# Optimization experiments

Measured on AMD Instinct MI355X. Metric: run time of the kernel, lower is better.

Reference implementation:

```python
import jax, jax.numpy as jnp
import numpy as np

B, F, D_IN, H, HEADS, NC = 2048, 64, 32, 128, 4, 16
EPG = 128            # random intra-graph edges per graph
N = B * F            # 131072 nodes
E = B * EPG          # 262144 edges (self-loops added in reference, like PyG GATConv)
LRELU_ATT = 0.2      # PyG GATConv negative_slope
LRELU_CLS = 0.01     # nn.LeakyReLU default


def setup_inputs() -> dict:
    key = jax.random.key(0)
    ks = jax.random.split(key, 24)
    emb = jax.random.normal(ks[0], (B, F, D_IN), jnp.float32)
    # per-graph random connectivity, offset so graphs are disjoint
    src_l = jax.random.randint(ks[1], (B, EPG), 0, F)
    tgt_l = jax.random.randint(ks[2], (B, EPG), 0, F)
    off = (jnp.arange(B) * F)[:, None]
    edge_index = jnp.stack([(src_l + off).reshape(-1), (tgt_l + off).reshape(-1)]).astype(jnp.int32)
    batch_idx = jnp.repeat(jnp.arange(B), F).astype(jnp.int32)
    s = 0.05
    return {
        'emb': emb, 'edge_index': edge_index, 'batch_idx': batch_idx,
        # fused aligner (single unique dim 32)
        'W_align': s * jax.random.normal(ks[3], (D_IN, H), jnp.float32),
        'b_align': jnp.zeros((H,), jnp.float32),
        'gate_logits': jnp.full((F,), 2.2, jnp.float32),
        # GATConv 1: in=H, out=H per head, heads=4, concat
        'W1': s * jax.random.normal(ks[4], (H, HEADS * H), jnp.float32),
        'a_src1': s * jax.random.normal(ks[5], (HEADS, H), jnp.float32),
        'a_dst1': s * jax.random.normal(ks[6], (HEADS, H), jnp.float32),
        'b1': jnp.zeros((HEADS * H,), jnp.float32),
        # GATConv 2: in=HEADS*H, out=H, heads=1, concat=False
        'W2': s * jax.random.normal(ks[7], (HEADS * H, H), jnp.float32),
        'a_src2': s * jax.random.normal(ks[8], (1, H), jnp.float32),
        'a_dst2': s * jax.random.normal(ks[9], (1, H), jnp.float32),
        'b2': jnp.zeros((H,), jnp.float32),
        # classifier MLP
        'Wc1': s * jax.random.normal(ks[10], (H, H // 2), jnp.float32),
        'bc1': jnp.zeros((H // 2,), jnp.float32),
        'Wc2': s * jax.random.normal(ks[11], (H // 2, NC), jnp.float32),
        'bc2': jnp.zeros((NC,), jnp.float32),
    }


def gat_layer(x, src, tgt, W, a_src, a_dst, b, concat):
    heads, dout = a_src.shape
    n = x.shape[0]
    h = (x @ W).reshape(n, heads, dout)                       # [N,h,d]
    e = jax.nn.leaky_relu(jnp.einsum('nhd,hd->nh', h, a_src)[src]
                          + jnp.einsum('nhd,hd->nh', h, a_dst)[tgt], LRELU_ATT)  # [E,h]
    m = jax.ops.segment_max(e, tgt, num_segments=n)           # segment softmax over in-neighbors
    p = jnp.exp(e - m[tgt])
    ssum = jax.ops.segment_sum(p, tgt, num_segments=n)
    alpha = p / (ssum[tgt] + 1e-16)
    out = jax.ops.segment_sum(h[src] * alpha[:, :, None], tgt, num_segments=n)
    out = out.reshape(n, heads * dout) if concat else out.mean(axis=1)
    return out + b


def reference(emb, edge_index, batch_idx, W_align, b_align, gate_logits,
              W1, a_src1, a_dst1, b1, W2, a_src2, a_dst2, b2, Wc1, bc1, Wc2, bc2):
    n = emb.shape[0] * emb.shape[1]
    aligned = emb @ W_align + b_align                         # fused align: [B,F,H]
    gate = jax.nn.sigmoid(gate_logits)                        # [F]
    x = (aligned * gate[None, :, None]).reshape(n, -1)        # gated node features [N,H]
    # add self-loops (GATConv default), eval mode -> dropout is identity
    loops = jnp.arange(n, dtype=edge_index.dtype)
    src = jnp.concatenate([edge_index[0], loops])
    tgt = jnp.concatenate([edge_index[1], loops])
    x = gat_layer(x, src, tgt, W1, a_src1, a_dst1, b1, True)  # [N, 4*H]
    x = jax.nn.elu(x)
    x = gat_layer(x, src, tgt, W2, a_src2, a_dst2, b2, False) # [N, H]
    gsum = jax.ops.segment_sum(x, batch_idx, num_segments=B)  # global_mean_pool
    cnt = jax.ops.segment_sum(jnp.ones((n, 1), x.dtype), batch_idx, num_segments=B)
    g = gsum / cnt                                            # [B, H]
    hc = jax.nn.leaky_relu(g @ Wc1 + bc1, LRELU_CLS)
    logits = hc @ Wc2 + bc2                                   # [B, NC]
    return logits, gate
```

## Files before the change

### kernel.cpp

```cpp
#include <hip/hip_runtime.h>
#include <math.h>

#define BLK 256

constexpr int Bg    = 2048;
constexpr int Fn    = 64;
constexpr int DIN   = 32;
constexpr int Hd    = 128;
constexpr int HEADS = 4;
constexpr int NC    = 16;
constexpr int EPG   = 128;
constexpr int Etot  = Bg * EPG;
constexpr int W1C   = HEADS * Hd;
constexpr int NSTR  = 68;
constexpr int EROW  = 136;
constexpr int PROW  = 68;
constexpr int NE    = EPG + Fn;

typedef __attribute__((ext_vector_type(8))) __bf16 bf16x8;
typedef __attribute__((ext_vector_type(4))) __bf16 bf16x4;
typedef __attribute__((ext_vector_type(4))) float  f32x4;

__device__ __align__(16) __bf16 g_wcombT[W1C * DIN];
__device__ float g_c1[W1C];
__device__ float g_c1s[16];
__device__ __align__(16) __bf16 g_w1F[HEADS*8*64*8];
__device__ __align__(16) __bf16 g_w2F[HEADS*4*8*64*8];
__device__ __align__(16) __bf16 g_wscF[HEADS*4*64*8];
__device__ __align__(16) __bf16 g_bs1F[64*8];

__global__ __launch_bounds__(BLK) void prep1(
    const float* __restrict__ Wa, const float* __restrict__ ba,
    const float* __restrict__ W1)
{
  __shared__ float WaS[DIN * Hd];
  const int tid = threadIdx.x;
  for (int i = tid; i < DIN * Hd; i += BLK) {
    int k = i >> 7, m = i & 127;
    WaS[m * DIN + k] = Wa[i];
  }
  __syncthreads();

  int i = blockIdx.x * BLK + tid;
  if (i < DIN * W1C) {
    int k = i & 31, n = i >> 5;
    float a0 = 0.f, a1 = 0.f, a2 = 0.f, a3 = 0.f;
    #pragma unroll
    for (int m = 0; m < Hd; m += 4) {
      a0 += WaS[(m  )*DIN + k] * W1[(m  )*W1C + n];
      a1 += WaS[(m+1)*DIN + k] * W1[(m+1)*W1C + n];
      a2 += WaS[(m+2)*DIN + k] * W1[(m+2)*W1C + n];
      a3 += WaS[(m+3)*DIN + k] * W1[(m+3)*W1C + n];
    }
    g_wcombT[i] = (__bf16)(a0 + a1 + a2 + a3);
  } else if (i < DIN*W1C + W1C) {
    int n = i - DIN*W1C;
    float a0 = 0.f, a1 = 0.f, a2 = 0.f, a3 = 0.f;
    #pragma unroll
    for (int m = 0; m < Hd; m += 4) {
      a0 += ba[m  ] * W1[(m  )*W1C + n];
      a1 += ba[m+1] * W1[(m+1)*W1C + n];
      a2 += ba[m+2] * W1[(m+2)*W1C + n];
      a3 += ba[m+3] * W1[(m+3)*W1C + n];
    }
    g_c1[n] = a0 + a1 + a2 + a3;
  }
}

constexpr int R_W2F  = 65536;
constexpr int R_W1F  = 16384;
constexpr int R_WSCZ = 8192;
constexpr int R_WSCD = 4096;
constexpr int R_BS1Z = 512;
constexpr int R_BS1D = 1024;
constexpr int R_C1S  = 128;
constexpr int B0 = R_W2F;
constexpr int B1 = B0 + R_W1F;
constexpr int B2 = B1 + R_WSCZ;
constexpr int B3 = B2 + R_WSCD;
constexpr int B4 = B3 + R_BS1Z;
constexpr int B5 = B4 + R_BS1D;
constexpr int P2_TOT = B5 + R_C1S;

__global__ __launch_bounds__(BLK) void prep2(
    const float* __restrict__ W2,
    const float* __restrict__ as1, const float* __restrict__ ad1,
    const float* __restrict__ as2, const float* __restrict__ ad2)
{
  int i = blockIdx.x * BLK + threadIdx.x;
  if (i < B0) {
    int k = i >> 7, n = i & 127;
    int hh = k >> 7, Ks = (k >> 5) & 3, q = (k >> 3) & 3, j = k & 7;
    int Nt = n >> 4, l = n & 15;
    int idx = (((hh*4 + Ks)*8 + Nt)*64 + (q*16 + l))*8 + j;
    g_w2F[idx] = (__bf16)W2[i];
  } else if (i < B1) {
    int j = i - B0;
    int jj = j & 7, lane = (j >> 3) & 63, T = j >> 9;
    int hh = T >> 3, Nt = T & 7;
    int q = lane >> 4, l = lane & 15;
    g_w1F[j] = g_wcombT[(hh*Hd + Nt*16 + l)*DIN + q*8 + jj];
  } else if (i < B2) {
    int j = i - B1;
    int lane = (j >> 3) & 63, c = lane & 15;
    if (c >= 2) g_wscF[j] = (__bf16)0.f;
  } else if (i < B3) {
    int j = i - B2;
    int p = j & 3, c = (j >> 2) & 1, k = j >> 3;
    const float* av = c ? ad2 : as2;
    float a0 = 0.f, a1 = 0.f, a2 = 0.f, a3 = 0.f;
    #pragma unroll
    for (int q = 0; q < 32; q += 4) {
      int f = p*32 + q;
      a0 += W2[(size_t)k*Hd + f    ] * av[f    ];
      a1 += W2[(size_t)k*Hd + f + 1] * av[f + 1];
      a2 += W2[(size_t)k*Hd + f + 2] * av[f + 2];
      a3 += W2[(size_t)k*Hd + f + 3] * av[f + 3];
    }
    float a = a0 + a1 + a2 + a3;
    a += __shfl_xor(a, 1);
    a += __shfl_xor(a, 2);
    if (p == 0) {
      int T = k >> 5, q2 = (k >> 3) & 3, jj = k & 7;
      g_wscF[(T*64 + q2*16 + c)*8 + jj] = (__bf16)a;
    }
  } else if (i < B4) {
    int j = i - B3;
    int lane = j >> 3, c = lane & 15;
    if (c >= 8) g_bs1F[j] = (__bf16)0.f;
  } else if (i < B5) {
    int j = i - B4;
    int p = j & 3, c = (j >> 2) & 7, kk = j >> 5;
    int h = c >> 1;
    const float* av = (c & 1) ? (ad1 + h*Hd) : (as1 + h*Hd);
    float a0 = 0.f, a1 = 0.f, a2 = 0.f, a3 = 0.f;
    #pragma unroll
    for (int q = 0; q < 32; q += 4) {
      int f = p*32 + q;
      a0 += (float)g_wcombT[(h*Hd + f    )*DIN + kk] * av[f    ];
      a1 += (float)g_wcombT[(h*Hd + f + 1)*DIN + kk] * av[f + 1];
      a2 += (float)g_wcombT[(h*Hd + f + 2)*DIN + kk] * av[f + 2];
      a3 += (float)g_wcombT[(h*Hd + f + 3)*DIN + kk] * av[f + 3];
    }
    float a = a0 + a1 + a2 + a3;
    a += __shfl_xor(a, 1);
    a += __shfl_xor(a, 2);
    if (p == 0) {
      int q2 = kk >> 3, jj = kk & 7;
      g_bs1F[(q2*16 + c)*8 + jj] = (__bf16)a;
    }
  } else if (i < P2_TOT) {
    int j = i - B5;
    int p = j & 7, c = j >> 3;
    float a = 0.f;
    if (c < 8) {
      int h = c >> 1;
      const float* av = (c & 1) ? (ad1 + h*Hd) : (as1 + h*Hd);
      #pragma unroll
      for (int q = 0; q < 16; ++q) {
        int f = p*16 + q;
        a += g_c1[h*Hd + f] * av[f];
      }
    }
    a += __shfl_xor(a, 1);
    a += __shfl_xor(a, 2);
    a += __shfl_xor(a, 4);
    if (p == 0) g_c1s[c] = a;
  }
}

__global__ __launch_bounds__(BLK, 3) void gat_main(
    const float* __restrict__ emb, const int* __restrict__ ei,
    const float* __restrict__ gate_logits,
    const float* __restrict__ b1, const float* __restrict__ b2,
    const float* __restrict__ Wc1, const float* __restrict__ bc1,
    const float* __restrict__ Wc2, const float* __restrict__ bc2,
    float* __restrict__ out)
{
  __shared__ __align__(16) __bf16 hT[Hd * NSTR];
  __shared__ __align__(16) __bf16 eluS[Fn * EROW];
  __shared__ __align__(16) __bf16 Pbf[Fn * PROW];
  __shared__ float sS1s[HEADS][Fn], sS1d[HEADS][Fn];
  __shared__ float sSrc[Fn], sDst[Fn], sSum[Fn], gateS[Fn];
  __shared__ float gpool[Hd], hcS[Fn];
  __shared__ __align__(16) __bf16 wS[Fn];

  unsigned* cells = (unsigned*)eluS;

  const int b    = blockIdx.x;
  const int tid  = threadIdx.x;
  const int lane = tid & 63;
  const int wv   = tid >> 6;
  const int quad = lane >> 4;
  const int l15  = lane & 15;
  const int nodeBase = wv * 16;
  const int m0   = wv * 32;
  const int base = b * Fn;

  const f32x4 zero4 = {0.f, 0.f, 0.f, 0.f};

  int es = 0, et = 0, ecell = 0;
  if (tid < NE) {
    if (tid < EPG) {
      es = ei[(size_t)b*EPG + tid] - base;
      et = ei[(size_t)Etot + (size_t)b*EPG + tid] - base;
    } else {
      es = et = tid - EPG;
    }
    ecell = et * Fn + es;
  }
  #pragma unroll
  for (int i = 0; i < 16; ++i) cells[tid + i*BLK] = 0u;
  {
    float4* p4 = (float4*)Pbf;
    const float4 z4 = {0.f,0.f,0.f,0.f};
    p4[tid] = z4; p4[tid + 256] = z4;
    if (tid < 32) p4[tid + 512] = z4;
  }
  if (tid < Fn) {
    float g = 1.f / (1.f + expf(-gate_logits[tid]));
    gateS[tid] = g; sSum[tid] = 0.f;
    if (b == 0) out[Bg*NC + tid] = g;
  }
  bf16x8 Af;
  {
    const float* ar = emb + ((size_t)base + nodeBase + l15) * DIN + quad * 8;
    float4 e0 = *(const float4*)ar;
    float4 e1 = *(const float4*)(ar + 4);
    Af[0]=(__bf16)e0.x; Af[1]=(__bf16)e0.y; Af[2]=(__bf16)e0.z; Af[3]=(__bf16)e0.w;
    Af[4]=(__bf16)e1.x; Af[5]=(__bf16)e1.y; Af[6]=(__bf16)e1.z; Af[7]=(__bf16)e1.w;
  }
  __syncthreads();

  bool rep = false;
  if (tid < NE) rep = (atomicAdd(&cells[ecell], 1u) == 0u);
  {
    bf16x8 Bs = *(const bf16x8*)(g_bs1F + lane*8);
    f32x4 ds = __builtin_amdgcn_mfma_f32_16x16x32_bf16(Af, Bs, zero4, 0, 0, 0);
    if (l15 < 8) {
      const float cc = g_c1s[l15];
      const int h = l15 >> 1;
      float* dstArr = (l15 & 1) ? &sS1d[h][0] : &sS1s[h][0];
      #pragma unroll
      for (int r = 0; r < 4; ++r) {
        int m = nodeBase + quad*4 + r;
        dstArr[m] = gateS[m] * (ds[r] + cc);
      }
    }
  }
  __syncthreads();

  float fm = 0.f;
  if (tid < NE && rep) fm = (float)cells[ecell];

  float gq[4];
  #pragma unroll
  for (int r = 0; r < 4; ++r) gq[r] = gateS[nodeBase + quad*4 + r];

  f32x4 acc[8];
  #pragma unroll
  for (int i = 0; i < 8; ++i) acc[i] = zero4;
  f32x4 accS = zero4;

  for (int hh = 0; hh < HEADS; ++hh) {
    #pragma unroll
    for (int Nt = 0; Nt < 8; ++Nt) {
      const int n = Nt*16 + l15;
      bf16x8 Bf = *(const bf16x8*)(g_w1F + ((hh*8 + Nt)*64 + lane)*8);
      f32x4 d = __builtin_amdgcn_mfma_f32_16x16x32_bf16(Af, Bf, zero4, 0, 0, 0);
      const float c1v = g_c1[hh*Hd + n];
      bf16x4 hw;
      #pragma unroll
      for (int r = 0; r < 4; ++r) hw[r] = (__bf16)((d[r] + c1v) * gq[r]);
      *(bf16x4*)(hT + n*NSTR + nodeBase + quad*4) = hw;
    }
    if (tid < NE && rep) {
      float e = sS1s[hh][es] + sS1d[hh][et];
      e = (e > 0.f) ? e : 0.2f * e;
      float pe = fm * __expf(e);
      Pbf[et*PROW + es] = (__bf16)pe;
      atomicAdd(&sSum[et], pe);
    }
    __syncthreads();

    {
      bf16x8 Ac[2][2];
      #pragma unroll
      for (int Mi = 0; Mi < 2; ++Mi)
        #pragma unroll
        for (int Ks = 0; Ks < 2; ++Ks)
          Ac[Mi][Ks] = *(const bf16x8*)(hT + (m0 + Mi*16 + l15)*NSTR + Ks*32 + quad*8);
      float4 b1v[2];
      #pragma unroll
      for (int Mi = 0; Mi < 2; ++Mi)
        b1v[Mi] = *(const float4*)&b1[hh*Hd + m0 + Mi*16 + quad*4];
      #pragma unroll
      for (int Nt = 0; Nt < 4; ++Nt) {
        bf16x8 B0f = *(const bf16x8*)(Pbf + (Nt*16 + l15)*PROW + quad*8);
        bf16x8 B1f = *(const bf16x8*)(Pbf + (Nt*16 + l15)*PROW + 32 + quad*8);
        const int t = Nt*16 + l15;
        const float si = 1.f / (sSum[t] + 1e-16f);
        #pragma unroll
        for (int Mi = 0; Mi < 2; ++Mi) {
          f32x4 d = __builtin_amdgcn_mfma_f32_16x16x32_bf16(Ac[Mi][0], B0f, zero4, 0, 0, 0);
          d = __builtin_amdgcn_mfma_f32_16x16x32_bf16(Ac[Mi][1], B1f, d, 0, 0, 0);
          bf16x4 w;
          #pragma unroll
          for (int r = 0; r < 4; ++r) {
            float hv = d[r]*si + b1v[Mi][r];
            hv = (hv > 0.f) ? hv : (__expf(hv) - 1.f);
            w[r] = (__bf16)hv;
          }
          *(bf16x4*)(eluS + t*EROW + m0 + Mi*16 + quad*4) = w;
        }
      }
    }
    __syncthreads();

    #pragma unroll
    for (int Ks = 0; Ks < 4; ++Ks) {
      bf16x8 A2 = *(const bf16x8*)(eluS + (nodeBase + l15)*EROW + Ks*32 + quad*8);
      #pragma unroll
      for (int Nt = 0; Nt < 8; ++Nt) {
        bf16x8 B2 = *(const bf16x8*)(g_w2F + (((hh*4 + Ks)*8 + Nt)*64 + lane)*8);
        acc[Nt] = __builtin_amdgcn_mfma_f32_16x16x32_bf16(A2, B2, acc[Nt], 0, 0, 0);
      }
      bf16x8 Bs2 = *(const bf16x8*)(g_wscF + ((hh*4 + Ks)*64 + lane)*8);
      accS = __builtin_amdgcn_mfma_f32_16x16x32_bf16(A2, Bs2, accS, 0, 0, 0);
    }
    {
      float4* p4 = (float4*)Pbf;
      const float4 z4 = {0.f,0.f,0.f,0.f};
      p4[tid] = z4; p4[tid + 256] = z4;
      if (tid < 32) p4[tid + 512] = z4;
      if (tid < Fn) sSum[tid] = 0.f;
    }
    __syncthreads();
  }

  #pragma unroll
  for (int Nt = 0; Nt < 8; ++Nt) {
    const int n = Nt*16 + l15;
    bf16x4 hw;
    #pragma unroll
    for (int r = 0; r < 4; ++r) hw[r] = (__bf16)acc[Nt][r];
    *(bf16x4*)(hT + n*NSTR + nodeBase + quad*4) = hw;
  }
  if (l15 == 0) {
    #pragma unroll
    for (int r = 0; r < 4; ++r) sSrc[nodeBase + quad*4 + r] = accS[r];
  } else if (l15 == 1) {
    #pragma unroll
    for (int r = 0; r < 4; ++r) sDst[nodeBase + quad*4 + r] = accS[r];
  }
  __syncthreads();

  if (tid < NE && rep) {
    float e = sSrc[es] + sDst[et];
    e = (e > 0.f) ? e : 0.2f * e;
    float pe = fm * __expf(e);
    Pbf[et*PROW + es] = (__bf16)pe;
    atomicAdd(&sSum[et], pe);
  }
  __syncthreads();

  {
    const int s_ = tid >> 2, part = tid & 3;
    float a = 0.f;
    #pragma unroll
    for (int q = 0; q < 16; ++q) {
      const int t = part*16 + q;
      a += (1.f / (sSum[t] + 1e-16f)) * (float)Pbf[t*PROW + s_];
    }
    a += __shfl_xor(a, 1);
    a += __shfl_xor(a, 2);
    if (part == 0) wS[s_] = (__bf16)(a * (1.f/64.f));
  }
  __syncthreads();

  {
    #pragma unroll
    for (int Mi = 0; Mi < 2; ++Mi) {
      f32x4 d = zero4;
      #pragma unroll
      for (int Ks = 0; Ks < 2; ++Ks) {
        bf16x8 A = *(const bf16x8*)(hT + (m0 + Mi*16 + l15)*NSTR + Ks*32 + quad*8);
        bf16x8 Bw = *(const bf16x8*)(wS + Ks*32 + quad*8);
        d = __builtin_amdgcn_mfma_f32_16x16x32_bf16(A, Bw, d, 0, 0, 0);
      }
      if (l15 == 0) {
        #pragma unroll
        for (int r = 0; r < 4; ++r) {
          const int f = m0 + Mi*16 + quad*4 + r;
          gpool[f] = d[r] + b2[f];
        }
      }
    }
  }
  __syncthreads();

  {
    const int c = tid >> 2, p = tid & 3;
    float a = 0.f;
    #pragma unroll
    for (int i = 0; i < 32; ++i) {
      const int k = p*32 + i;
      a += gpool[k] * Wc1[k*Fn + c];
    }
    a += __shfl_xor(a, 1);
    a += __shfl_xor(a, 2);
    if (p == 0) {
      a += bc1[c];
      hcS[c] = (a > 0.f) ? a : 0.01f * a;
    }
  }
  __syncthreads();

  {
    const int c = tid >> 4, p = tid & 15;
    float a = 0.f;
    #pragma unroll
    for (int i = 0; i < 4; ++i) {
      const int k = p*4 + i;
      a += hcS[k] * Wc2[k*NC + c];
    }
    a += __shfl_xor(a, 1);
    a += __shfl_xor(a, 2);
    a += __shfl_xor(a, 4);
    a += __shfl_xor(a, 8);
    if (p == 0) out[b*NC + c] = a + bc2[c];
  }
}

extern "C" void kernel_launch(void* const* d_in, const int* in_sizes, int n_in,
                              void* d_out, int out_size, void* d_ws, size_t ws_size,
                              hipStream_t stream) {
  const float* emb = (const float*)d_in[0];
  const int*   ei  = (const int*)  d_in[1];
  const float* Wa  = (const float*)d_in[3];
  const float* ba  = (const float*)d_in[4];
  const float* gl  = (const float*)d_in[5];
  const float* W1  = (const float*)d_in[6];
  const float* as1 = (const float*)d_in[7];
  const float* ad1 = (const float*)d_in[8];
  const float* b1  = (const float*)d_in[9];
  const float* W2  = (const float*)d_in[10];
  const float* as2 = (const float*)d_in[11];
  const float* ad2 = (const float*)d_in[12];
  const float* b2  = (const float*)d_in[13];
  const float* Wc1 = (const float*)d_in[14];
  const float* bc1 = (const float*)d_in[15];
  const float* Wc2 = (const float*)d_in[16];
  const float* bc2 = (const float*)d_in[17];
  float* out = (float*)d_out;

  const int prep1N = DIN*W1C + W1C;
  hipLaunchKernelGGL(prep1, dim3((prep1N + BLK - 1)/BLK), dim3(BLK), 0, stream,
                     Wa, ba, W1);
  hipLaunchKernelGGL(prep2, dim3((P2_TOT + BLK - 1)/BLK), dim3(BLK), 0, stream,
                     W2, as1, ad1, as2, ad2);
  hipLaunchKernelGGL(gat_main, dim3(Bg), dim3(BLK), 0, stream,
                     emb, ei, gl, b1, b2, Wc1, bc1, Wc2, bc2, out);
}
```

Measured before the change: 190.4 us.

## Merge prep kernels and make each wave own its nodes in layer-1 aggregation

```diff
diff --git a/kernel.cpp b/kernel.cpp
--- a/kernel.cpp
+++ b/kernel.cpp
@@ -24,27 +24,40 @@
 __device__ __align__(16) __bf16 g_wcombT[W1C * DIN];
 __device__ float g_c1[W1C];
 __device__ float g_c1s[16];
-__device__ __align__(16) __bf16 g_w1F[HEADS*8*64*8];
 __device__ __align__(16) __bf16 g_w2F[HEADS*4*8*64*8];
 __device__ __align__(16) __bf16 g_wscF[HEADS*4*64*8];
 __device__ __align__(16) __bf16 g_bs1F[64*8];
 
-__global__ __launch_bounds__(BLK) void prep1(
+constexpr int N_WC   = DIN * W1C;
+constexpr int C0 = N_WC;
+constexpr int C1 = C0 + W1C;
+constexpr int C2 = C1 + HEADS*4*8*64*8;
+constexpr int C3 = C2 + HEADS*4*64*8;
+constexpr int C4 = C3 + 4096;
+constexpr int C5 = C4 + 512;
+constexpr int C6 = C5 + 8192;
+constexpr int CP_TOT = C6 + 256;
+
+__global__ __launch_bounds__(BLK) void prep(
     const float* __restrict__ Wa, const float* __restrict__ ba,
-    const float* __restrict__ W1)
+    const float* __restrict__ W1, const float* __restrict__ W2,
+    const float* __restrict__ as1, const float* __restrict__ ad1,
+    const float* __restrict__ as2, const float* __restrict__ ad2)
 {
   __shared__ float WaS[DIN * Hd];
   const int tid = threadIdx.x;
-  for (int i = tid; i < DIN * Hd; i += BLK) {
-    int k = i >> 7, m = i & 127;
-    WaS[m * DIN + k] = Wa[i];
-  }
-  __syncthreads();
+  if (blockIdx.x < 64) {
+    for (int i2 = tid; i2 < DIN * Hd; i2 += BLK) {
+      int k = i2 >> 7, m = i2 & 127;
+      WaS[m * DIN + k] = Wa[i2];
+    }
+    __syncthreads();
+  }
 
   int i = blockIdx.x * BLK + tid;
-  if (i < DIN * W1C) {
+  if (i < C0) {
     int k = i & 31, n = i >> 5;
-    float a0 = 0.f, a1 = 0.f, a2 = 0.f, a3 = 0.f;
+    float a0=0.f,a1=0.f,a2=0.f,a3=0.f;
     #pragma unroll
     for (int m = 0; m < Hd; m += 4) {
       a0 += WaS[(m  )*DIN + k] * W1[(m  )*W1C + n];
@@ -52,10 +65,10 @@
       a2 += WaS[(m+2)*DIN + k] * W1[(m+2)*W1C + n];
       a3 += WaS[(m+3)*DIN + k] * W1[(m+3)*W1C + n];
     }
-    g_wcombT[i] = (__bf16)(a0 + a1 + a2 + a3);
-  } else if (i < DIN*W1C + W1C) {
-    int n = i - DIN*W1C;
-    float a0 = 0.f, a1 = 0.f, a2 = 0.f, a3 = 0.f;
+    g_wcombT[i] = (__bf16)(a0+a1+a2+a3);
+  } else if (i < C1) {
+    int n = i - C0;
+    float a0=0.f,a1=0.f,a2=0.f,a3=0.f;
     #pragma unroll
     for (int m = 0; m < Hd; m += 4) {
       a0 += ba[m  ] * W1[(m  )*W1C + n];
@@ -63,52 +76,23 @@
       a2 += ba[m+2] * W1[(m+2)*W1C + n];
       a3 += ba[m+3] * W1[(m+3)*W1C + n];
     }
-    g_c1[n] = a0 + a1 + a2 + a3;
-  }
-}
-
-constexpr int R_W2F  = 65536;
-constexpr int R_W1F  = 16384;
-constexpr int R_WSCZ = 8192;
-constexpr int R_WSCD = 4096;
-constexpr int R_BS1Z = 512;
-constexpr int R_BS1D = 1024;
-constexpr int R_C1S  = 128;
-constexpr int B0 = R_W2F;
-constexpr int B1 = B0 + R_W1F;
-constexpr int B2 = B1 + R_WSCZ;
-constexpr int B3 = B2 + R_WSCD;
-constexpr int B4 = B3 + R_BS1Z;
-constexpr int B5 = B4 + R_BS1D;
-constexpr int P2_TOT = B5 + R_C1S;
-
-__global__ __launch_bounds__(BLK) void prep2(
-    const float* __restrict__ W2,
-    const float* __restrict__ as1, const float* __restrict__ ad1,
-    const float* __restrict__ as2, const float* __restrict__ ad2)
-{
-  int i = blockIdx.x * BLK + threadIdx.x;
-  if (i < B0) {
-    int k = i >> 7, n = i & 127;
-    int hh = k >> 7, Ks = (k >> 5) & 3, q = (k >> 3) & 3, j = k & 7;
+    g_c1[n] = a0+a1+a2+a3;
+  } else if (i < C2) {
+    int j = i - C1;
+    int k = j >> 7, n = j & 127;
+    int hh = k >> 7, Ks = (k >> 5) & 3, q = (k >> 3) & 3, jj = k & 7;
     int Nt = n >> 4, l = n & 15;
-    int idx = (((hh*4 + Ks)*8 + Nt)*64 + (q*16 + l))*8 + j;
-    g_w2F[idx] = (__bf16)W2[i];
-  } else if (i < B1) {
-    int j = i - B0;
-    int jj = j & 7, lane = (j >> 3) & 63, T = j >> 9;
-    int hh = T >> 3, Nt = T & 7;
-    int q = lane >> 4, l = lane & 15;
-    g_w1F[j] = g_wcombT[(hh*Hd + Nt*16 + l)*DIN + q*8 + jj];
-  } else if (i < B2) {
-    int j = i - B1;
+    int idx = (((hh*4 + Ks)*8 + Nt)*64 + (q*16 + l))*8 + jj;
+    g_w2F[idx] = (__bf16)W2[j];
+  } else if (i < C3) {
+    int j = i - C2;
     int lane = (j >> 3) & 63, c = lane & 15;
     if (c >= 2) g_wscF[j] = (__bf16)0.f;
-  } else if (i < B3) {
-    int j = i - B2;
+  } else if (i < C4) {
+    int j = i - C3;
     int p = j & 3, c = (j >> 2) & 1, k = j >> 3;
     const float* av = c ? ad2 : as2;
-    float a0 = 0.f, a1 = 0.f, a2 = 0.f, a3 = 0.f;
+    float a0=0.f,a1=0.f,a2=0.f,a3=0.f;
     #pragma unroll
     for (int q = 0; q < 32; q += 4) {
       int f = p*32 + q;
@@ -117,55 +101,65 @@
       a2 += W2[(size_t)k*Hd + f + 2] * av[f + 2];
       a3 += W2[(size_t)k*Hd + f + 3] * av[f + 3];
     }
-    float a = a0 + a1 + a2 + a3;
+    float a = a0+a1+a2+a3;
     a += __shfl_xor(a, 1);
     a += __shfl_xor(a, 2);
     if (p == 0) {
       int T = k >> 5, q2 = (k >> 3) & 3, jj = k & 7;
       g_wscF[(T*64 + q2*16 + c)*8 + jj] = (__bf16)a;
     }
-  } else if (i < B4) {
-    int j = i - B3;
+  } else if (i < C5) {
+    int j = i - C4;
     int lane = j >> 3, c = lane & 15;
     if (c >= 8) g_bs1F[j] = (__bf16)0.f;
-  } else if (i < B5) {
-    int j = i - B4;
-    int p = j & 3, c = (j >> 2) & 7, kk = j >> 5;
+  } else if (i < C6) {
+    int j = i - C5;
+    int p = j & 31, c = (j >> 5) & 7, kk = j >> 8;
     int h = c >> 1;
     const float* av = (c & 1) ? (ad1 + h*Hd) : (as1 + h*Hd);
-    float a0 = 0.f, a1 = 0.f, a2 = 0.f, a3 = 0.f;
-    #pragma unroll
-    for (int q = 0; q < 32; q += 4) {
-      int f = p*32 + q;
-      a0 += (float)g_wcombT[(h*Hd + f    )*DIN + kk] * av[f    ];
-      a1 += (float)g_wcombT[(h*Hd + f + 1)*DIN + kk] * av[f + 1];
-      a2 += (float)g_wcombT[(h*Hd + f + 2)*DIN + kk] * av[f + 2];
-      a3 += (float)g_wcombT[(h*Hd + f + 3)*DIN + kk] * av[f + 3];
-    }
-    float a = a0 + a1 + a2 + a3;
-    a += __shfl_xor(a, 1);
-    a += __shfl_xor(a, 2);
+    float acc = 0.f;
+    #pragma unroll
+    for (int mi = 0; mi < 4; ++mi) {
+      int m = p*4 + mi;
+      float t0=0.f,t1=0.f,t2=0.f,t3=0.f;
+      #pragma unroll
+      for (int f = 0; f < Hd; f += 4) {
+        t0 += W1[m*W1C + h*Hd + f    ] * av[f    ];
+        t1 += W1[m*W1C + h*Hd + f + 1] * av[f + 1];
+        t2 += W1[m*W1C + h*Hd + f + 2] * av[f + 2];
+        t3 += W1[m*W1C + h*Hd + f + 3] * av[f + 3];
+      }
+      acc += Wa[kk*Hd + m] * (t0+t1+t2+t3);
+    }
+    acc += __shfl_xor(acc, 1);
+    acc += __shfl_xor(acc, 2);
+    acc += __shfl_xor(acc, 4);
+    acc += __shfl_xor(acc, 8);
+    acc += __shfl_xor(acc, 16);
     if (p == 0) {
       int q2 = kk >> 3, jj = kk & 7;
-      g_bs1F[(q2*16 + c)*8 + jj] = (__bf16)a;
-    }
-  } else if (i < P2_TOT) {
-    int j = i - B5;
-    int p = j & 7, c = j >> 3;
-    float a = 0.f;
-    if (c < 8) {
-      int h = c >> 1;
-      const float* av = (c & 1) ? (ad1 + h*Hd) : (as1 + h*Hd);
-      #pragma unroll
-      for (int q = 0; q < 16; ++q) {
-        int f = p*16 + q;
-        a += g_c1[h*Hd + f] * av[f];
-      }
-    }
-    a += __shfl_xor(a, 1);
-    a += __shfl_xor(a, 2);
-    a += __shfl_xor(a, 4);
-    if (p == 0) g_c1s[c] = a;
+      g_bs1F[(q2*16 + c)*8 + jj] = (__bf16)acc;
+    }
+  } else if (i < CP_TOT) {
+    int j = i - C6;
+    int p = j & 31, c = j >> 5;
+    int h = c >> 1;
+    const float* av = (c & 1) ? (ad1 + h*Hd) : (as1 + h*Hd);
+    float acc = 0.f;
+    #pragma unroll
+    for (int mi = 0; mi < 4; ++mi) {
+      int m = p*4 + mi;
+      float t = 0.f;
+      #pragma unroll
+      for (int f = 0; f < Hd; ++f) t += W1[m*W1C + h*Hd + f] * av[f];
+      acc += ba[m] * t;
+    }
+    acc += __shfl_xor(acc, 1);
+    acc += __shfl_xor(acc, 2);
+    acc += __shfl_xor(acc, 4);
+    acc += __shfl_xor(acc, 8);
+    acc += __shfl_xor(acc, 16);
+    if (p == 0) g_c1s[c] = acc;
   }
 }
 
@@ -262,11 +256,13 @@
   for (int i = 0; i < 8; ++i) acc[i] = zero4;
   f32x4 accS = zero4;
 
+  const int myT = nodeBase + l15;
+
   for (int hh = 0; hh < HEADS; ++hh) {
     #pragma unroll
     for (int Nt = 0; Nt < 8; ++Nt) {
       const int n = Nt*16 + l15;
-      bf16x8 Bf = *(const bf16x8*)(g_w1F + ((hh*8 + Nt)*64 + lane)*8);
+      bf16x8 Bf = *(const bf16x8*)(g_wcombT + (hh*Hd + n)*DIN + quad*8);
       f32x4 d = __builtin_amdgcn_mfma_f32_16x16x32_bf16(Af, Bf, zero4, 0, 0, 0);
       const float c1v = g_c1[hh*Hd + n];
       bf16x4 hw;
@@ -284,56 +280,44 @@
     __syncthreads();
 
     {
-      bf16x8 Ac[2][2];
-      #pragma unroll
-      for (int Mi = 0; Mi < 2; ++Mi)
+      const float si = 1.f / (sSum[myT] + 1e-16f);
+      bf16x8 Bp0 = *(const bf16x8*)(Pbf + myT*PROW + quad*8);
+      bf16x8 Bp1 = *(const bf16x8*)(Pbf + myT*PROW + 32 + quad*8);
+      #pragma unroll
+      for (int Mi = 0; Mi < 8; ++Mi) {
+        bf16x8 A0 = *(const bf16x8*)(hT + (Mi*16 + l15)*NSTR + quad*8);
+        bf16x8 A1 = *(const bf16x8*)(hT + (Mi*16 + l15)*NSTR + 32 + quad*8);
+        f32x4 d = __builtin_amdgcn_mfma_f32_16x16x32_bf16(A0, Bp0, zero4, 0, 0, 0);
+        d = __builtin_amdgcn_mfma_f32_16x16x32_bf16(A1, Bp1, d, 0, 0, 0);
+        float4 bv = *(const float4*)&b1[hh*Hd + Mi*16 + quad*4];
+        bf16x4 w;
         #pragma unroll
-        for (int Ks = 0; Ks < 2; ++Ks)
-          Ac[Mi][Ks] = *(const bf16x8*)(hT + (m0 + Mi*16 + l15)*NSTR + Ks*32 + quad*8);
-      float4 b1v[2];
-      #pragma unroll
-      for (int Mi = 0; Mi < 2; ++Mi)
-        b1v[Mi] = *(const float4*)&b1[hh*Hd + m0 + Mi*16 + quad*4];
-      #pragma unroll
-      for (int Nt = 0; Nt < 4; ++Nt) {
-        bf16x8 B0f = *(const bf16x8*)(Pbf + (Nt*16 + l15)*PROW + quad*8);
-        bf16x8 B1f = *(const bf16x8*)(Pbf + (Nt*16 + l15)*PROW + 32 + quad*8);
-        const int t = Nt*16 + l15;
-        const float si = 1.f / (sSum[t] + 1e-16f);
+        for (int r = 0; r < 4; ++r) {
+          float hv = d[r]*si + bv[r];
+          hv = (hv > 0.f) ? hv : (__expf(hv) - 1.f);
+          w[r] = (__bf16)hv;
+        }
+        *(bf16x4*)(eluS + myT*EROW + Mi*16 + quad*4) = w;
+      }
+      #pragma unroll
+      for (int Ks = 0; Ks < 4; ++Ks) {
+        bf16x8 A2 = *(const bf16x8*)(eluS + myT*EROW + Ks*32 + quad*8);
         #pragma unroll
-        for (int Mi = 0; Mi < 2; ++Mi) {
-          f32x4 d = __builtin_amdgcn_mfma_f32_16x16x32_bf16(Ac[Mi][0], B0f, zero4, 0, 0, 0);
-          d = __builtin_amdgcn_mfma_f32_16x16x32_bf16(Ac[Mi][1], B1f, d, 0, 0, 0);
-          bf16x4 w;
-          #pragma unroll
-          for (int r = 0; r < 4; ++r) {
-            float hv = d[r]*si + b1v[Mi][r];
-            hv = (hv > 0.f) ? hv : (__expf(hv) - 1.f);
-            w[r] = (__bf16)hv;
-          }
-          *(bf16x4*)(eluS + t*EROW + m0 + Mi*16 + quad*4) = w;
+        for (int Nt = 0; Nt < 8; ++Nt) {
+          bf16x8 B2 = *(const bf16x8*)(g_w2F + (((hh*4 + Ks)*8 + Nt)*64 + lane)*8);
+          acc[Nt] = __builtin_amdgcn_mfma_f32_16x16x32_bf16(A2, B2, acc[Nt], 0, 0, 0);
         }
-      }
-    }
-    __syncthreads();
-
-    #pragma unroll
-    for (int Ks = 0; Ks < 4; ++Ks) {
-      bf16x8 A2 = *(const bf16x8*)(eluS + (nodeBase + l15)*EROW + Ks*32 + quad*8);
-      #pragma unroll
-      for (int Nt = 0; Nt < 8; ++Nt) {
-        bf16x8 B2 = *(const bf16x8*)(g_w2F + (((hh*4 + Ks)*8 + Nt)*64 + lane)*8);
-        acc[Nt] = __builtin_amdgcn_mfma_f32_16x16x32_bf16(A2, B2, acc[Nt], 0, 0, 0);
-      }
-      bf16x8 Bs2 = *(const bf16x8*)(g_wscF + ((hh*4 + Ks)*64 + lane)*8);
-      accS = __builtin_amdgcn_mfma_f32_16x16x32_bf16(A2, Bs2, accS, 0, 0, 0);
-    }
-    {
-      float4* p4 = (float4*)Pbf;
-      const float4 z4 = {0.f,0.f,0.f,0.f};
-      p4[tid] = z4; p4[tid + 256] = z4;
-      if (tid < 32) p4[tid + 512] = z4;
-      if (tid < Fn) sSum[tid] = 0.f;
+        bf16x8 Bs2 = *(const bf16x8*)(g_wscF + ((hh*4 + Ks)*64 + lane)*8);
+        accS = __builtin_amdgcn_mfma_f32_16x16x32_bf16(A2, Bs2, accS, 0, 0, 0);
+      }
+      {
+        bf16x8 z8;
+        #pragma unroll
+        for (int j = 0; j < 8; ++j) z8[j] = (__bf16)0.f;
+        *(bf16x8*)(Pbf + myT*PROW + quad*16) = z8;
+        *(bf16x8*)(Pbf + myT*PROW + quad*16 + 8) = z8;
+        if (quad == 0) sSum[myT] = 0.f;
+      }
     }
     __syncthreads();
   }
@@ -454,11 +438,8 @@
   const float* bc2 = (const float*)d_in[17];
   float* out = (float*)d_out;
 
-  const int prep1N = DIN*W1C + W1C;
-  hipLaunchKernelGGL(prep1, dim3((prep1N + BLK - 1)/BLK), dim3(BLK), 0, stream,
-                     Wa, ba, W1);
-  hipLaunchKernelGGL(prep2, dim3((P2_TOT + BLK - 1)/BLK), dim3(BLK), 0, stream,
-                     W2, as1, ad1, as2, ad2);
+  hipLaunchKernelGGL(prep, dim3((CP_TOT + BLK - 1)/BLK), dim3(BLK), 0, stream,
+                     Wa, ba, W1, W2, as1, ad1, as2, ad2);
   hipLaunchKernelGGL(gat_main, dim3(Bg), dim3(BLK), 0, stream,
                      emb, ei, gl, b1, b2, Wc1, bc1, Wc2, bc2, out);
 }
```

New measurement: 236.9 us. 1.24x slower.
